# Performance work log

Measured on AMD Instinct MI355X. Metric: run time of the kernel, lower is better.

## Reference

```python
import jax, jax.numpy as jnp
import numpy as np

B, N, K = 4096, 87, 87


def setup_inputs() -> dict:
    key = jax.random.key(0)
    ks = jax.random.split(key, 6)
    x = jax.random.normal(ks[0], (B, N, N), dtype=jnp.float32)
    evals = jax.random.uniform(ks[1], (B, K), dtype=jnp.float32)
    evecs = jax.random.normal(ks[2], (B, N, K), dtype=jnp.float32)
    # learned per-node diffusion times (torch inits to 0, clamped to 1e-8;
    # use small positive values to exercise the exp decay)
    diffusion_time = jax.random.uniform(ks[3], (N,), dtype=jnp.float32) * 0.1
    # MiniMLP: single Linear(2*N -> N)
    lim = 1.0 / np.sqrt(2 * N)
    W = jax.random.uniform(ks[4], (N, 2 * N), minval=-lim, maxval=lim, dtype=jnp.float32)
    b = jax.random.uniform(ks[5], (N,), minval=-lim, maxval=lim, dtype=jnp.float32)
    return {"x": x, "evals": evals, "evecs": evecs,
            "diffusion_time": diffusion_time, "W": W, "b": b}


def reference(x, evals, evecs, diffusion_time, W, b):
    # clamp diffusion times (torch does this in-place on .data)
    t = jnp.maximum(diffusion_time, 1e-8)                     # (N,)
    # expa[b,i,m] = exp(-t_i * eval[b,m])
    expa = jnp.exp(-t[None, :, None] * evals[:, None, :])     # (B,N,K)
    # kernel[b,i,j] = sum_m evec[b,i,m] * expa[b,i,m] * evec[b,j,m]
    # (equivalent to the diag_embed + triple matmul + diagonal in the torch code)
    kernel = jnp.einsum('bim,bjm->bij', evecs * expa, evecs)  # (B,N,N)
    x_diffuse = jnp.concatenate([x, kernel], axis=2)          # (B,N,2N)
    return x_diffuse @ W.T + b                                # (B,N,N)
```

## Files before the change

kernel.cpp:

```cpp
#include <hip/hip_runtime.h>
#include <hip/hip_bf16.h>
#include <math.h>

#define NN    87
#define NN2   (NN * NN)
#define RP    96
#define SW    128
#define WPH   104
#define WPANEL (RP * WPH)
#define NT    256

#define WS_NEED (2 * WPANEL * 2)

typedef __attribute__((ext_vector_type(8))) short bf16x8;
typedef __attribute__((ext_vector_type(4))) short bf16x4;
typedef __attribute__((ext_vector_type(4))) float f32x4;
typedef float f32x4u __attribute__((ext_vector_type(4), aligned(4)));

__device__ __forceinline__ short f2bf(float f) {
    __hip_bfloat16 h = __float2bfloat16(f);
    return *(short*)&h;
}
__device__ __forceinline__ float bf2f(short s) {
    union { unsigned u; float f; } v;
    v.u = ((unsigned)(unsigned short)s) << 16;
    return v.f;
}

__device__ __forceinline__ int swz(int row, int col) {
    int m = ((row & 7) << 3) | (((row >> 3) & 1) << 2);
    return row * SW + (col ^ m);
}

__global__ void prep(const float* __restrict__ W, short* __restrict__ wp) {
    int idx = (int)blockIdx.x * NT + (int)threadIdx.x;
    if (idx >= 2 * WPANEL) return;
    int p = idx / WPANEL, rem = idx - p * WPANEL;
    int r = rem / WPH, c = rem - r * WPH;
    short v = 0;
    if (r < NN && c < NN) v = f2bf(W[r * (2 * NN) + p * NN + c]);
    wp[idx] = v;
}

template <bool WS>
__device__ __forceinline__ bf16x8 wload(const short* __restrict__ wp,
                                        const float* __restrict__ gW,
                                        int panel, int jrow, int jcl, int k0, bool tailKs)
{
    if constexpr (WS) {
        return *(const bf16x8*)&wp[panel * WPANEL + jrow * WPH + k0];
    } else {
        float v[8];
        if (!tailKs) {
            f32x4u a  = *(const f32x4u*)(gW + jcl * (2 * NN) + panel * NN + k0);
            f32x4u b4 = *(const f32x4u*)(gW + jcl * (2 * NN) + panel * NN + k0 + 4);
            v[0] = a.x; v[1] = a.y; v[2] = a.z; v[3] = a.w;
            v[4] = b4.x; v[5] = b4.y; v[6] = b4.z; v[7] = b4.w;
        } else {
            #pragma unroll
            for (int q = 0; q < 8; ++q) {
                int k = k0 + q;
                v[q] = (k < NN) ? gW[jcl * (2 * NN) + panel * NN + k] : 0.f;
            }
        }
        bf16x8 o;
        #pragma unroll
        for (int q = 0; q < 8; ++q) o[q] = f2bf(v[q]);
        return o;
    }
}

template <bool WS>
__global__ __launch_bounds__(NT, 3)
void fused(const float* __restrict__ gx, const float* __restrict__ gevals,
           const float* __restrict__ gevecs, const float* __restrict__ dtime,
           const float* __restrict__ gW, const float* __restrict__ bias,
           const short* __restrict__ wp, float* __restrict__ out)
{
    __shared__ __align__(16) short smem[2 * RP * SW];
    short* const sE = smem;
    short* const sX = smem + RP * SW;
    short* const sD = smem;
    float* const sF = (float*)smem;
    __shared__ float sLam[RP];

    const int b    = (int)blockIdx.x;
    const int tid  = (int)threadIdx.x;
    const int lane = tid & 63;
    const int wave = tid >> 6;
    const int l15  = lane & 15;
    const int lk   = lane >> 4;
    const int i0   = (wave >> 1) * 48;
    const int j0   = (wave & 1) * 48;

    const float* __restrict__ Eb   = gevecs + (size_t)b * NN2;
    const float* __restrict__ xb   = gx     + (size_t)b * NN2;
    const float* __restrict__ lamb = gevals + (size_t)b * NN;

    if (tid < RP) sLam[tid] = (tid < NN) ? lamb[tid] : 0.f;

    int ir[3], jr[3];
    float tr_[3];
    #pragma unroll
    for (int r = 0; r < 3; ++r) {
        ir[r] = i0 + 16 * r + l15;
        jr[r] = j0 + 16 * r + l15;
        tr_[r] = fmaxf(dtime[ir[r] < NN ? ir[r] : NN - 1], 1e-8f);
    }

    bf16x8 wfx[3][3];
    #pragma unroll
    for (int ks = 0; ks < 3; ++ks)
        #pragma unroll
        for (int wr = 0; wr < 3; ++wr) {
            int jc = jr[wr] < NN ? jr[wr] : NN - 1;
            wfx[ks][wr] = wload<WS>(wp, gW, 0, jr[wr], jc, ks * 32 + lk * 8, ks == 2);
        }

    for (int u = tid; u < NN * 22; u += NT) {
        int r = u / 22, sg = u - r * 22, c = sg * 4;
        const float* pE = Eb + r * NN + c;
        const float* pX = xb + r * NN + c;
        float e0, e1, e2, e3, x0, x1, x2, x3;
        if (sg < 21) {
            f32x4u te = *(const f32x4u*)pE; e0 = te.x; e1 = te.y; e2 = te.z; e3 = te.w;
            f32x4u tx = *(const f32x4u*)pX; x0 = tx.x; x1 = tx.y; x2 = tx.z; x3 = tx.w;
        } else {
            e0 = pE[0]; e1 = pE[1]; e2 = pE[2]; e3 = 0.f;
            x0 = pX[0]; x1 = pX[1]; x2 = pX[2]; x3 = 0.f;
        }
        bf16x4 we = {f2bf(e0), f2bf(e1), f2bf(e2), f2bf(e3)};
        bf16x4 wx = {f2bf(x0), f2bf(x1), f2bf(x2), f2bf(x3)};
        *(bf16x4*)&sE[swz(r, c)] = we;
        *(bf16x4*)&sX[swz(r, c)] = wx;
    }
    {
        const bf16x4 z = {0, 0, 0, 0};
        for (int u = tid; u < 9 * 24; u += NT) {
            int r = NN + u / 24, c = (u % 24) * 4;
            *(bf16x4*)&sE[swz(r, c)] = z;
            *(bf16x4*)&sX[swz(r, c)] = z;
        }
        for (int u = tid; u < NN * 2; u += NT) {
            int r = u >> 1, c = 88 + (u & 1) * 4;
            *(bf16x4*)&sE[swz(r, c)] = z;
            *(bf16x4*)&sX[swz(r, c)] = z;
        }
    }
    __syncthreads();

    f32x4 acc1[3][3];
    #pragma unroll
    for (int c = 0; c < 3; ++c)
        #pragma unroll
        for (int r = 0; r < 3; ++r) acc1[c][r] = (f32x4){0.f, 0.f, 0.f, 0.f};

    #pragma unroll
    for (int ks = 0; ks < 3; ++ks) {
        const int k0 = ks * 32 + lk * 8;
        f32x4 la  = *(const f32x4*)&sLam[k0];
        f32x4 lb4 = *(const f32x4*)&sLam[k0 + 4];
        float l8_[8] = {la.x, la.y, la.z, la.w, lb4.x, lb4.y, lb4.z, lb4.w};

        bf16x8 ef[3], af[3];
        #pragma unroll
        for (int c = 0; c < 3; ++c) {
            bf16x4 lo = *(const bf16x4*)&sE[swz(jr[c], k0)];
            bf16x4 hi = *(const bf16x4*)&sE[swz(jr[c], k0 + 4)];
            #pragma unroll
            for (int q = 0; q < 4; ++q) { ef[c][q] = lo[q]; ef[c][q + 4] = hi[q]; }
        }
        #pragma unroll
        for (int r = 0; r < 3; ++r) {
            bf16x4 lo = *(const bf16x4*)&sE[swz(ir[r], k0)];
            bf16x4 hi = *(const bf16x4*)&sE[swz(ir[r], k0 + 4)];
            #pragma unroll
            for (int q = 0; q < 4; ++q) {
                af[r][q]     = f2bf(bf2f(lo[q]) * __expf(-tr_[r] * l8_[q]));
                af[r][q + 4] = f2bf(bf2f(hi[q]) * __expf(-tr_[r] * l8_[q + 4]));
            }
        }
        #pragma unroll
        for (int c = 0; c < 3; ++c)
            #pragma unroll
            for (int r = 0; r < 3; ++r)
                acc1[c][r] = __builtin_amdgcn_mfma_f32_16x16x32_bf16(ef[c], af[r], acc1[c][r], 0, 0, 0);
    }
    __syncthreads();

    bf16x8 wfd[3][3];
    #pragma unroll
    for (int ks = 0; ks < 3; ++ks)
        #pragma unroll
        for (int wr = 0; wr < 3; ++wr) {
            int jc = jr[wr] < NN ? jr[wr] : NN - 1;
            wfd[ks][wr] = wload<WS>(wp, gW, 1, jr[wr], jc, ks * 32 + lk * 8, ks == 2);
        }

    #pragma unroll
    for (int c = 0; c < 3; ++c) {
        const int jb = j0 + 16 * c + lk * 4;
        #pragma unroll
        for (int r = 0; r < 3; ++r) {
            const int i = i0 + 16 * r + l15;
            bf16x4 v = {f2bf(acc1[c][r][0]), f2bf(acc1[c][r][1]),
                        f2bf(acc1[c][r][2]), f2bf(acc1[c][r][3])};
            *(bf16x4*)&sD[swz(i, jb)] = v;
        }
    }
    __builtin_amdgcn_sched_barrier(0);

    f32x4 acc2[3][3];
    #pragma unroll
    for (int wr = 0; wr < 3; ++wr)
        #pragma unroll
        for (int xc = 0; xc < 3; ++xc) acc2[wr][xc] = (f32x4){0.f, 0.f, 0.f, 0.f};

    #pragma unroll
    for (int ks = 0; ks < 3; ++ks) {
        const int k0 = ks * 32 + lk * 8;
        bf16x8 xf[3];
        #pragma unroll
        for (int xc = 0; xc < 3; ++xc) {
            bf16x4 lo = *(const bf16x4*)&sX[swz(ir[xc], k0)];
            bf16x4 hi = *(const bf16x4*)&sX[swz(ir[xc], k0 + 4)];
            #pragma unroll
            for (int q = 0; q < 4; ++q) { xf[xc][q] = lo[q]; xf[xc][q + 4] = hi[q]; }
        }
        #pragma unroll
        for (int wr = 0; wr < 3; ++wr)
            #pragma unroll
            for (int xc = 0; xc < 3; ++xc)
                acc2[wr][xc] = __builtin_amdgcn_mfma_f32_16x16x32_bf16(wfx[ks][wr], xf[xc], acc2[wr][xc], 0, 0, 0);
    }
    __syncthreads();

    #pragma unroll
    for (int ks = 0; ks < 3; ++ks) {
        const int k0 = ks * 32 + lk * 8;
        bf16x8 df[3];
        #pragma unroll
        for (int xc = 0; xc < 3; ++xc) {
            bf16x4 lo = *(const bf16x4*)&sD[swz(ir[xc], k0)];
            bf16x4 hi = *(const bf16x4*)&sD[swz(ir[xc], k0 + 4)];
            #pragma unroll
            for (int q = 0; q < 4; ++q) { df[xc][q] = lo[q]; df[xc][q + 4] = hi[q]; }
        }
        #pragma unroll
        for (int wr = 0; wr < 3; ++wr)
            #pragma unroll
            for (int xc = 0; xc < 3; ++xc)
                acc2[wr][xc] = __builtin_amdgcn_mfma_f32_16x16x32_bf16(wfd[ks][wr], df[xc], acc2[wr][xc], 0, 0, 0);
    }
    __syncthreads();

    #pragma unroll
    for (int wr = 0; wr < 3; ++wr) {
        const int jb = j0 + 16 * wr + lk * 4;
        float bj[4];
        if (jb + 3 < NN) {
            f32x4u t = *(const f32x4u*)(bias + jb);
            bj[0] = t.x; bj[1] = t.y; bj[2] = t.z; bj[3] = t.w;
        } else {
            #pragma unroll
            for (int q = 0; q < 4; ++q) bj[q] = (jb + q < NN) ? bias[jb + q] : 0.f;
        }
        #pragma unroll
        for (int xc = 0; xc < 3; ++xc) {
            const int i = i0 + 16 * xc + l15;
            #pragma unroll
            for (int q = 0; q < 4; ++q) {
                const int j = jb + q;
                if (j < NN) sF[i * NN + j] = acc2[wr][xc][q] + bj[q];
            }
        }
    }
    __syncthreads();

    {
        float* __restrict__ gb = out + (size_t)b * NN2;
        const int s = (4 - ((b * NN2) & 3)) & 3;
        if (tid < s) gb[tid] = sF[tid];
        const int C = (NN2 - s) >> 2;
        for (int m = tid; m < C; m += NT) {
            const int n = s + 4 * m;
            f32x4 v;
            v.x = sF[n]; v.y = sF[n + 1]; v.z = sF[n + 2]; v.w = sF[n + 3];
            *(f32x4*)(gb + n) = v;
        }
        const int tl = s + 4 * C;
        if (tid < NN2 - tl) gb[tl + tid] = sF[tl + tid];
    }
}

extern "C" void kernel_launch(void* const* d_in, const int* in_sizes, int n_in,
                              void* d_out, int out_size, void* d_ws, size_t ws_size,
                              hipStream_t stream)
{
    const float* x     = (const float*)d_in[0];
    const float* evals = (const float*)d_in[1];
    const float* evecs = (const float*)d_in[2];
    const float* dtime = (const float*)d_in[3];
    const float* W     = (const float*)d_in[4];
    const float* bias  = (const float*)d_in[5];
    float* out = (float*)d_out;

    const int B = in_sizes[1] / NN;

    if (ws_size >= (size_t)WS_NEED) {
        short* wp = (short*)d_ws;
        prep<<<(2 * WPANEL + NT - 1) / NT, NT, 0, stream>>>(W, wp);
        fused<true><<<dim3(B), dim3(NT), 0, stream>>>(x, evals, evecs, dtime, W, bias, wp, out);
    } else {
        fused<false><<<dim3(B), dim3(NT), 0, stream>>>(x, evals, evecs, dtime, W, bias, nullptr, out);
    }
}
```

Baseline: 106.1 us.

## Stream evecs directly into LDS as fp32 and overlap x loads with GEMM

```diff
diff --git a/kernel.cpp b/kernel.cpp
--- a/kernel.cpp
+++ b/kernel.cpp
@@ -4,13 +4,18 @@
 
 #define NN    87
 #define NN2   (NN * NN)
-#define RP    96
-#define SW    128
+#define EPW   92
+#define EPN   (96 * EPW + 4)
+#define XPW   92
+#define XPN   (96 * XPW + 16)
 #define WPH   104
-#define WPANEL (RP * WPH)
+#define WPANEL (96 * WPH)
 #define NT    256
 
-#define WS_NEED (2 * WPANEL * 2)
+#define WS_W     0
+#define WS_EPAD  (2 * WPANEL * 2)
+#define EPAD_N   8360
+#define WS_NEED  (WS_EPAD + EPAD_N * 4)
 
 typedef __attribute__((ext_vector_type(8))) short bf16x8;
 typedef __attribute__((ext_vector_type(4))) short bf16x4;
@@ -21,25 +26,29 @@
     __hip_bfloat16 h = __float2bfloat16(f);
     return *(short*)&h;
 }
-__device__ __forceinline__ float bf2f(short s) {
-    union { unsigned u; float f; } v;
-    v.u = ((unsigned)(unsigned short)s) << 16;
-    return v.f;
-}
-
-__device__ __forceinline__ int swz(int row, int col) {
-    int m = ((row & 7) << 3) | (((row >> 3) & 1) << 2);
-    return row * SW + (col ^ m);
-}
-
-__global__ void prep(const float* __restrict__ W, short* __restrict__ wp) {
+
+__device__ __forceinline__ void gl16(const float* g, float* l) {
+    __builtin_amdgcn_global_load_lds(
+        (const __attribute__((address_space(1))) void*)g,
+        (__attribute__((address_space(3))) void*)l, 16, 0, 0);
+}
+
+__global__ void prep(const float* __restrict__ W, const float* __restrict__ evecs,
+                     int B, char* __restrict__ ws)
+{
     int idx = (int)blockIdx.x * NT + (int)threadIdx.x;
-    if (idx >= 2 * WPANEL) return;
-    int p = idx / WPANEL, rem = idx - p * WPANEL;
-    int r = rem / WPH, c = rem - r * WPH;
-    short v = 0;
-    if (r < NN && c < NN) v = f2bf(W[r * (2 * NN) + p * NN + c]);
-    wp[idx] = v;
+    short* wp = (short*)(ws + WS_W);
+    float* ep = (float*)(ws + WS_EPAD);
+    if (idx < 2 * WPANEL) {
+        int p = idx / WPANEL, rem = idx - p * WPANEL;
+        int r = rem / WPH, c = rem - r * WPH;
+        short v = 0;
+        if (r < NN && c < NN) v = f2bf(W[r * (2 * NN) + p * NN + c]);
+        wp[idx] = v;
+    }
+    int i2 = idx - 2 * WPANEL;
+    if (i2 >= 0 && i2 < EPAD_N)
+        ep[i2] = (i2 < NN2) ? evecs[(size_t)(B - 1) * NN2 + i2] : 0.f;
 }
 
 template <bool WS>
@@ -75,14 +84,13 @@
 void fused(const float* __restrict__ gx, const float* __restrict__ gevals,
            const float* __restrict__ gevecs, const float* __restrict__ dtime,
            const float* __restrict__ gW, const float* __restrict__ bias,
-           const short* __restrict__ wp, float* __restrict__ out)
+           const char* __restrict__ ws, int B, float* __restrict__ out)
 {
-    __shared__ __align__(16) short smem[2 * RP * SW];
-    short* const sE = smem;
-    short* const sX = smem + RP * SW;
-    short* const sD = smem;
-    float* const sF = (float*)smem;
-    __shared__ float sLam[RP];
+    __shared__ __align__(16) float sE[EPN];
+    __shared__ __align__(16) short sX[XPN];
+    __shared__ float sLam[96];
+    short* const sD = (short*)sE;
+    float* const sF = (float*)sE;
 
     const int b    = (int)blockIdx.x;
     const int tid  = (int)threadIdx.x;
@@ -93,11 +101,15 @@
     const int i0   = (wave >> 1) * 48;
     const int j0   = (wave & 1) * 48;
 
-    const float* __restrict__ Eb   = gevecs + (size_t)b * NN2;
-    const float* __restrict__ xb   = gx     + (size_t)b * NN2;
-    const float* __restrict__ lamb = gevals + (size_t)b * NN;
-
-    if (tid < RP) sLam[tid] = (tid < NN) ? lamb[tid] : 0.f;
+    const float* __restrict__ Eb = gevecs + (size_t)b * NN2;
+    const float* __restrict__ xb = gx     + (size_t)b * NN2;
+    const short* wp = nullptr;
+    if constexpr (WS) {
+        wp = (const short*)(ws + WS_W);
+        if (b == B - 1) Eb = (const float*)(ws + WS_EPAD);
+    }
+
+    if (tid < 96) sLam[tid] = (tid < NN) ? gevals[(size_t)b * NN + tid] : 3e38f;
 
     int ir[3], jr[3];
     float tr_[3];
@@ -108,46 +120,62 @@
         tr_[r] = fmaxf(dtime[ir[r] < NN ? ir[r] : NN - 1], 1e-8f);
     }
 
-    bf16x8 wfx[3][3];
-    #pragma unroll
-    for (int ks = 0; ks < 3; ++ks)
-        #pragma unroll
-        for (int wr = 0; wr < 3; ++wr) {
-            int jc = jr[wr] < NN ? jr[wr] : NN - 1;
-            wfx[ks][wr] = wload<WS>(wp, gW, 0, jr[wr], jc, ks * 32 + lk * 8, ks == 2);
-        }
-
-    for (int u = tid; u < NN * 22; u += NT) {
-        int r = u / 22, sg = u - r * 22, c = sg * 4;
-        const float* pE = Eb + r * NN + c;
-        const float* pX = xb + r * NN + c;
-        float e0, e1, e2, e3, x0, x1, x2, x3;
-        if (sg < 21) {
-            f32x4u te = *(const f32x4u*)pE; e0 = te.x; e1 = te.y; e2 = te.z; e3 = te.w;
-            f32x4u tx = *(const f32x4u*)pX; x0 = tx.x; x1 = tx.y; x2 = tx.z; x3 = tx.w;
-        } else {
-            e0 = pE[0]; e1 = pE[1]; e2 = pE[2]; e3 = 0.f;
-            x0 = pX[0]; x1 = pX[1]; x2 = pX[2]; x3 = 0.f;
-        }
-        bf16x4 we = {f2bf(e0), f2bf(e1), f2bf(e2), f2bf(e3)};
-        bf16x4 wx = {f2bf(x0), f2bf(x1), f2bf(x2), f2bf(x3)};
-        *(bf16x4*)&sE[swz(r, c)] = we;
-        *(bf16x4*)&sX[swz(r, c)] = wx;
-    }
-    {
-        const bf16x4 z = {0, 0, 0, 0};
-        for (int u = tid; u < 9 * 24; u += NT) {
-            int r = NN + u / 24, c = (u % 24) * 4;
-            *(bf16x4*)&sE[swz(r, c)] = z;
-            *(bf16x4*)&sX[swz(r, c)] = z;
-        }
-        for (int u = tid; u < NN * 2; u += NT) {
-            int r = u >> 1, c = 88 + (u & 1) * 4;
-            *(bf16x4*)&sE[swz(r, c)] = z;
-            *(bf16x4*)&sX[swz(r, c)] = z;
-        }
-    }
-    __syncthreads();
+    if (tid < 4)  sE[96 * EPW + tid] = 0.f;
+    if (tid < 16) sX[96 * XPW + tid] = 0;
+    for (int u = tid; u < 96 * 5; u += NT) {
+        int r = u / 5, c = NN + u % 5;
+        sX[r * XPW + c] = 0;
+    }
+    for (int u = tid; u < 9 * NN; u += NT) {
+        int r = NN + u / NN, c = u % NN;
+        sX[r * XPW + c] = 0;
+    }
+
+    if constexpr (WS) {
+        for (int vc = wave; vc < 35; vc += 4) {
+            int p  = vc * 256 + lane * 4;
+            int row = p / EPW;
+            int col = p - row * EPW;
+            const float* g = Eb + row * NN + col;
+            if (vc < 34) gl16(g, &sE[vc * 256]);
+            else if (lane < 32) gl16(g, &sE[vc * 256]);
+        }
+    } else {
+        for (int u = tid; u < NN * 22; u += NT) {
+            int r = u / 22, sg = u - r * 22, c = sg * 4;
+            const float* pE = Eb + r * NN + c;
+            if (sg < 21) *(f32x4*)&sE[r * EPW + c] = *(const f32x4u*)pE;
+            else { f32x4 t; t.x = pE[0]; t.y = pE[1]; t.z = pE[2]; t.w = 0.f;
+                   *(f32x4*)&sE[r * EPW + c] = t; }
+        }
+        for (int u = tid; u < 96 * 4; u += NT) {
+            int r = u >> 2, c = 88 + (u & 3);
+            sE[r * EPW + c] = 0.f;
+        }
+        for (int u = tid; u < 9 * 88; u += NT) {
+            int r = NN + u / 88, c = u % 88;
+            sE[r * EPW + c] = 0.f;
+        }
+    }
+
+    float xq[8][4];
+    float x7568 = 0.f;
+    #pragma unroll
+    for (int k = 0; k < 8; ++k) {
+        int u = tid + k * NT;
+        int uc = (u < 1892) ? u : 1891;
+        f32x4u t = *(const f32x4u*)(xb + 4 * uc);
+        xq[k][0] = t.x; xq[k][1] = t.y; xq[k][2] = t.z; xq[k][3] = t.w;
+    }
+    if (tid == 0) x7568 = xb[7568];
+
+    if constexpr (WS) {
+        asm volatile("s_waitcnt vmcnt(8) lgkmcnt(0)" ::: "memory");
+        __builtin_amdgcn_s_barrier();
+        __builtin_amdgcn_sched_barrier(0);
+    } else {
+        __syncthreads();
+    }
 
     f32x4 acc1[3][3];
     #pragma unroll
@@ -165,19 +193,19 @@
         bf16x8 ef[3], af[3];
         #pragma unroll
         for (int c = 0; c < 3; ++c) {
-            bf16x4 lo = *(const bf16x4*)&sE[swz(jr[c], k0)];
-            bf16x4 hi = *(const bf16x4*)&sE[swz(jr[c], k0 + 4)];
-            #pragma unroll
-            for (int q = 0; q < 4; ++q) { ef[c][q] = lo[q]; ef[c][q + 4] = hi[q]; }
+            f32x4 lo = *(const f32x4*)&sE[jr[c] * EPW + k0];
+            f32x4 hi = *(const f32x4*)&sE[jr[c] * EPW + k0 + 4];
+            #pragma unroll
+            for (int q = 0; q < 4; ++q) { ef[c][q] = f2bf(lo[q]); ef[c][q + 4] = f2bf(hi[q]); }
         }
         #pragma unroll
         for (int r = 0; r < 3; ++r) {
-            bf16x4 lo = *(const bf16x4*)&sE[swz(ir[r], k0)];
-            bf16x4 hi = *(const bf16x4*)&sE[swz(ir[r], k0 + 4)];
+            f32x4 lo = *(const f32x4*)&sE[ir[r] * EPW + k0];
+            f32x4 hi = *(const f32x4*)&sE[ir[r] * EPW + k0 + 4];
             #pragma unroll
             for (int q = 0; q < 4; ++q) {
-                af[r][q]     = f2bf(bf2f(lo[q]) * __expf(-tr_[r] * l8_[q]));
-                af[r][q + 4] = f2bf(bf2f(hi[q]) * __expf(-tr_[r] * l8_[q + 4]));
+                af[r][q]     = f2bf(lo[q] * __expf(-tr_[r] * l8_[q]));
+                af[r][q + 4] = f2bf(hi[q] * __expf(-tr_[r] * l8_[q + 4]));
             }
         }
         #pragma unroll
@@ -188,27 +216,49 @@
     }
     __syncthreads();
 
-    bf16x8 wfd[3][3];
+    #pragma unroll
+    for (int c = 0; c < 3; ++c) {
+        const int jb = j0 + 16 * c + lk * 4;
+        if (jb < 92) {
+            #pragma unroll
+            for (int r = 0; r < 3; ++r) {
+                const int i = i0 + 16 * r + l15;
+                bf16x4 v = {f2bf(acc1[c][r][0]), f2bf(acc1[c][r][1]),
+                            f2bf(acc1[c][r][2]), f2bf(acc1[c][r][3])};
+                *(bf16x4*)&sD[i * XPW + jb] = v;
+            }
+        }
+    }
+    if (tid < 4) sD[96 * XPW + tid] = 0;
+    __builtin_amdgcn_sched_barrier(0);
+
+    #pragma unroll
+    for (int k = 0; k < 8; ++k) {
+        int u = tid + k * NT;
+        if (u < 1892) {
+            int f = 4 * u;
+            #pragma unroll
+            for (int e = 0; e < 4; ++e) {
+                int fe = f + e;
+                if (fe < NN2) {
+                    int r = fe / NN, c = fe - r * NN;
+                    sX[r * XPW + c] = f2bf(xq[k][e]);
+                }
+            }
+        }
+    }
+    if (tid == 0) sX[86 * XPW + 86] = f2bf(x7568);
+
+    bf16x8 wfx[3][3], wfd[3][3];
     #pragma unroll
     for (int ks = 0; ks < 3; ++ks)
         #pragma unroll
         for (int wr = 0; wr < 3; ++wr) {
             int jc = jr[wr] < NN ? jr[wr] : NN - 1;
+            wfx[ks][wr] = wload<WS>(wp, gW, 0, jr[wr], jc, ks * 32 + lk * 8, ks == 2);
             wfd[ks][wr] = wload<WS>(wp, gW, 1, jr[wr], jc, ks * 32 + lk * 8, ks == 2);
         }
-
-    #pragma unroll
-    for (int c = 0; c < 3; ++c) {
-        const int jb = j0 + 16 * c + lk * 4;
-        #pragma unroll
-        for (int r = 0; r < 3; ++r) {
-            const int i = i0 + 16 * r + l15;
-            bf16x4 v = {f2bf(acc1[c][r][0]), f2bf(acc1[c][r][1]),
-                        f2bf(acc1[c][r][2]), f2bf(acc1[c][r][3])};
-            *(bf16x4*)&sD[swz(i, jb)] = v;
-        }
-    }
-    __builtin_amdgcn_sched_barrier(0);
+    __syncthreads();
 
     f32x4 acc2[3][3];
     #pragma unroll
@@ -222,8 +272,8 @@
         bf16x8 xf[3];
         #pragma unroll
         for (int xc = 0; xc < 3; ++xc) {
-            bf16x4 lo = *(const bf16x4*)&sX[swz(ir[xc], k0)];
-            bf16x4 hi = *(const bf16x4*)&sX[swz(ir[xc], k0 + 4)];
+            bf16x4 lo = *(const bf16x4*)&sX[ir[xc] * XPW + k0];
+            bf16x4 hi = *(const bf16x4*)&sX[ir[xc] * XPW + k0 + 4];
             #pragma unroll
             for (int q = 0; q < 4; ++q) { xf[xc][q] = lo[q]; xf[xc][q + 4] = hi[q]; }
         }
@@ -233,16 +283,14 @@
             for (int xc = 0; xc < 3; ++xc)
                 acc2[wr][xc] = __builtin_amdgcn_mfma_f32_16x16x32_bf16(wfx[ks][wr], xf[xc], acc2[wr][xc], 0, 0, 0);
     }
-    __syncthreads();
-
     #pragma unroll
     for (int ks = 0; ks < 3; ++ks) {
         const int k0 = ks * 32 + lk * 8;
         bf16x8 df[3];
         #pragma unroll
         for (int xc = 0; xc < 3; ++xc) {
-            bf16x4 lo = *(const bf16x4*)&sD[swz(ir[xc], k0)];
-            bf16x4 hi = *(const bf16x4*)&sD[swz(ir[xc], k0 + 4)];
+            bf16x4 lo = *(const bf16x4*)&sD[ir[xc] * XPW + k0];
+            bf16x4 hi = *(const bf16x4*)&sD[ir[xc] * XPW + k0 + 4];
             #pragma unroll
             for (int q = 0; q < 4; ++q) { df[xc][q] = lo[q]; df[xc][q + 4] = hi[q]; }
         }
@@ -308,10 +356,12 @@
     const int B = in_sizes[1] / NN;
 
     if (ws_size >= (size_t)WS_NEED) {
-        short* wp = (short*)d_ws;
-        prep<<<(2 * WPANEL + NT - 1) / NT, NT, 0, stream>>>(W, wp);
-        fused<true><<<dim3(B), dim3(NT), 0, stream>>>(x, evals, evecs, dtime, W, bias, wp, out);
+        const int prep_elems = 2 * WPANEL + EPAD_N;
+        prep<<<(prep_elems + NT - 1) / NT, NT, 0, stream>>>(W, evecs, B, (char*)d_ws);
+        fused<true><<<dim3(B), dim3(NT), 0, stream>>>(x, evals, evecs, dtime, W, bias,
+                                                      (const char*)d_ws, B, out);
     } else {
-        fused<false><<<dim3(B), dim3(NT), 0, stream>>>(x, evals, evecs, dtime, W, bias, nullptr, out);
-    }
-}
+        fused<false><<<dim3(B), dim3(NT), 0, stream>>>(x, evals, evecs, dtime, W, bias,
+                                                       nullptr, B, out);
+    }
+}
```

After: 96.00 us. 9.5% less time.

## Shrink LDS with padded unswizzled tiles, batch global loads, raise occupancy to 4

Applied to the files above, without the earlier changes.

```diff
diff --git a/kernel.cpp b/kernel.cpp
--- a/kernel.cpp
+++ b/kernel.cpp
@@ -4,10 +4,10 @@
 
 #define NN    87
 #define NN2   (NN * NN)
-#define RP    96
-#define SW    128
+#define PW    92
+#define PN    (96 * PW + 16)
 #define WPH   104
-#define WPANEL (RP * WPH)
+#define WPANEL (96 * WPH)
 #define NT    256
 
 #define WS_NEED (2 * WPANEL * 2)
@@ -25,11 +25,6 @@
     union { unsigned u; float f; } v;
     v.u = ((unsigned)(unsigned short)s) << 16;
     return v.f;
-}
-
-__device__ __forceinline__ int swz(int row, int col) {
-    int m = ((row & 7) << 3) | (((row >> 3) & 1) << 2);
-    return row * SW + (col ^ m);
 }
 
 __global__ void prep(const float* __restrict__ W, short* __restrict__ wp) {
@@ -71,18 +66,18 @@
 }
 
 template <bool WS>
-__global__ __launch_bounds__(NT, 3)
+__global__ __launch_bounds__(NT, 4)
 void fused(const float* __restrict__ gx, const float* __restrict__ gevals,
            const float* __restrict__ gevecs, const float* __restrict__ dtime,
            const float* __restrict__ gW, const float* __restrict__ bias,
            const short* __restrict__ wp, float* __restrict__ out)
 {
-    __shared__ __align__(16) short smem[2 * RP * SW];
+    __shared__ __align__(16) short smem[2 * PN];
     short* const sE = smem;
-    short* const sX = smem + RP * SW;
+    short* const sX = smem + PN;
     short* const sD = smem;
     float* const sF = (float*)smem;
-    __shared__ float sLam[RP];
+    __shared__ float sLam[96];
 
     const int b    = (int)blockIdx.x;
     const int tid  = (int)threadIdx.x;
@@ -93,11 +88,11 @@
     const int i0   = (wave >> 1) * 48;
     const int j0   = (wave & 1) * 48;
 
-    const float* __restrict__ Eb   = gevecs + (size_t)b * NN2;
-    const float* __restrict__ xb   = gx     + (size_t)b * NN2;
-    const float* __restrict__ lamb = gevals + (size_t)b * NN;
-
-    if (tid < RP) sLam[tid] = (tid < NN) ? lamb[tid] : 0.f;
+    const float* __restrict__ Eb = gevecs + (size_t)b * NN2;
+    const float* __restrict__ xb = gx     + (size_t)b * NN2;
+    const short* wpp = WS ? wp : nullptr;
+
+    if (tid < 96) sLam[tid] = (tid < NN) ? gevals[(size_t)b * NN + tid] : 3e38f;
 
     int ir[3], jr[3];
     float tr_[3];
@@ -108,43 +103,47 @@
         tr_[r] = fmaxf(dtime[ir[r] < NN ? ir[r] : NN - 1], 1e-8f);
     }
 
-    bf16x8 wfx[3][3];
-    #pragma unroll
-    for (int ks = 0; ks < 3; ++ks)
-        #pragma unroll
-        for (int wr = 0; wr < 3; ++wr) {
-            int jc = jr[wr] < NN ? jr[wr] : NN - 1;
-            wfx[ks][wr] = wload<WS>(wp, gW, 0, jr[wr], jc, ks * 32 + lk * 8, ks == 2);
-        }
-
-    for (int u = tid; u < NN * 22; u += NT) {
-        int r = u / 22, sg = u - r * 22, c = sg * 4;
+    float ve[8][4], vx[8][4];
+    #pragma unroll
+    for (int k = 0; k < 8; ++k) {
+        int u = tid + k * NT;
+        int uu = (u < 1914) ? u : 0;
+        int r = uu / 22, sg = uu - r * 22, c = sg * 4;
         const float* pE = Eb + r * NN + c;
         const float* pX = xb + r * NN + c;
-        float e0, e1, e2, e3, x0, x1, x2, x3;
         if (sg < 21) {
-            f32x4u te = *(const f32x4u*)pE; e0 = te.x; e1 = te.y; e2 = te.z; e3 = te.w;
-            f32x4u tx = *(const f32x4u*)pX; x0 = tx.x; x1 = tx.y; x2 = tx.z; x3 = tx.w;
+            f32x4u te = *(const f32x4u*)pE;
+            ve[k][0] = te.x; ve[k][1] = te.y; ve[k][2] = te.z; ve[k][3] = te.w;
+            f32x4u tx = *(const f32x4u*)pX;
+            vx[k][0] = tx.x; vx[k][1] = tx.y; vx[k][2] = tx.z; vx[k][3] = tx.w;
         } else {
-            e0 = pE[0]; e1 = pE[1]; e2 = pE[2]; e3 = 0.f;
-            x0 = pX[0]; x1 = pX[1]; x2 = pX[2]; x3 = 0.f;
-        }
-        bf16x4 we = {f2bf(e0), f2bf(e1), f2bf(e2), f2bf(e3)};
-        bf16x4 wx = {f2bf(x0), f2bf(x1), f2bf(x2), f2bf(x3)};
-        *(bf16x4*)&sE[swz(r, c)] = we;
-        *(bf16x4*)&sX[swz(r, c)] = wx;
-    }
+            ve[k][0] = pE[0]; ve[k][1] = pE[1]; ve[k][2] = pE[2]; ve[k][3] = 0.f;
+            vx[k][0] = pX[0]; vx[k][1] = pX[1]; vx[k][2] = pX[2]; vx[k][3] = 0.f;
+        }
+    }
+
     {
         const bf16x4 z = {0, 0, 0, 0};
-        for (int u = tid; u < 9 * 24; u += NT) {
-            int r = NN + u / 24, c = (u % 24) * 4;
-            *(bf16x4*)&sE[swz(r, c)] = z;
-            *(bf16x4*)&sX[swz(r, c)] = z;
-        }
-        for (int u = tid; u < NN * 2; u += NT) {
-            int r = u >> 1, c = 88 + (u & 1) * 4;
-            *(bf16x4*)&sE[swz(r, c)] = z;
-            *(bf16x4*)&sX[swz(r, c)] = z;
+        for (int u = tid; u < 596; u += NT) {
+            int p = u & 1, v = u >> 1;
+            short* P = p ? sX : sE;
+            int off;
+            if (v < 207)      { int r = 87 + v / 23, s = v % 23; off = r * PW + s * 4; }
+            else if (v < 294) { off = (v - 207) * PW + 88; }
+            else              { off = 96 * PW + (v - 294) * 4; }
+            *(bf16x4*)&P[off] = z;
+        }
+    }
+
+    #pragma unroll
+    for (int k = 0; k < 8; ++k) {
+        int u = tid + k * NT;
+        if (u < 1914) {
+            int r = u / 22, sg = u - r * 22, c = sg * 4;
+            bf16x4 we = {f2bf(ve[k][0]), f2bf(ve[k][1]), f2bf(ve[k][2]), f2bf(ve[k][3])};
+            bf16x4 wx = {f2bf(vx[k][0]), f2bf(vx[k][1]), f2bf(vx[k][2]), f2bf(vx[k][3])};
+            *(bf16x4*)&sE[r * PW + c] = we;
+            *(bf16x4*)&sX[r * PW + c] = wx;
         }
     }
     __syncthreads();
@@ -165,15 +164,15 @@
         bf16x8 ef[3], af[3];
         #pragma unroll
         for (int c = 0; c < 3; ++c) {
-            bf16x4 lo = *(const bf16x4*)&sE[swz(jr[c], k0)];
-            bf16x4 hi = *(const bf16x4*)&sE[swz(jr[c], k0 + 4)];
+            bf16x4 lo = *(const bf16x4*)&sE[jr[c] * PW + k0];
+            bf16x4 hi = *(const bf16x4*)&sE[jr[c] * PW + k0 + 4];
             #pragma unroll
             for (int q = 0; q < 4; ++q) { ef[c][q] = lo[q]; ef[c][q + 4] = hi[q]; }
         }
         #pragma unroll
         for (int r = 0; r < 3; ++r) {
-            bf16x4 lo = *(const bf16x4*)&sE[swz(ir[r], k0)];
-            bf16x4 hi = *(const bf16x4*)&sE[swz(ir[r], k0 + 4)];
+            bf16x4 lo = *(const bf16x4*)&sE[ir[r] * PW + k0];
+            bf16x4 hi = *(const bf16x4*)&sE[ir[r] * PW + k0 + 4];
             #pragma unroll
             for (int q = 0; q < 4; ++q) {
                 af[r][q]     = f2bf(bf2f(lo[q]) * __expf(-tr_[r] * l8_[q]));
@@ -188,27 +187,30 @@
     }
     __syncthreads();
 
-    bf16x8 wfd[3][3];
+    bf16x8 wfx[3][3];
     #pragma unroll
     for (int ks = 0; ks < 3; ++ks)
         #pragma unroll
         for (int wr = 0; wr < 3; ++wr) {
             int jc = jr[wr] < NN ? jr[wr] : NN - 1;
-            wfd[ks][wr] = wload<WS>(wp, gW, 1, jr[wr], jc, ks * 32 + lk * 8, ks == 2);
+            wfx[ks][wr] = wload<WS>(wpp, gW, 0, jr[wr], jc, ks * 32 + lk * 8, ks == 2);
         }
 
     #pragma unroll
     for (int c = 0; c < 3; ++c) {
         const int jb = j0 + 16 * c + lk * 4;
-        #pragma unroll
-        for (int r = 0; r < 3; ++r) {
-            const int i = i0 + 16 * r + l15;
-            bf16x4 v = {f2bf(acc1[c][r][0]), f2bf(acc1[c][r][1]),
-                        f2bf(acc1[c][r][2]), f2bf(acc1[c][r][3])};
-            *(bf16x4*)&sD[swz(i, jb)] = v;
+        if (jb < PW) {
+            #pragma unroll
+            for (int r = 0; r < 3; ++r) {
+                const int i = i0 + 16 * r + l15;
+                bf16x4 v = {f2bf(acc1[c][r][0]), f2bf(acc1[c][r][1]),
+                            f2bf(acc1[c][r][2]), f2bf(acc1[c][r][3])};
+                *(bf16x4*)&sD[i * PW + jb] = v;
+            }
         }
     }
     __builtin_amdgcn_sched_barrier(0);
+    __syncthreads();
 
     f32x4 acc2[3][3];
     #pragma unroll
@@ -222,8 +224,8 @@
         bf16x8 xf[3];
         #pragma unroll
         for (int xc = 0; xc < 3; ++xc) {
-            bf16x4 lo = *(const bf16x4*)&sX[swz(ir[xc], k0)];
-            bf16x4 hi = *(const bf16x4*)&sX[swz(ir[xc], k0 + 4)];
+            bf16x4 lo = *(const bf16x4*)&sX[ir[xc] * PW + k0];
+            bf16x4 hi = *(const bf16x4*)&sX[ir[xc] * PW + k0 + 4];
             #pragma unroll
             for (int q = 0; q < 4; ++q) { xf[xc][q] = lo[q]; xf[xc][q + 4] = hi[q]; }
         }
@@ -233,16 +235,19 @@
             for (int xc = 0; xc < 3; ++xc)
                 acc2[wr][xc] = __builtin_amdgcn_mfma_f32_16x16x32_bf16(wfx[ks][wr], xf[xc], acc2[wr][xc], 0, 0, 0);
     }
-    __syncthreads();
-
     #pragma unroll
     for (int ks = 0; ks < 3; ++ks) {
         const int k0 = ks * 32 + lk * 8;
-        bf16x8 df[3];
+        bf16x8 wfd[3], df[3];
+        #pragma unroll
+        for (int wr = 0; wr < 3; ++wr) {
+            int jc = jr[wr] < NN ? jr[wr] : NN - 1;
+            wfd[wr] = wload<WS>(wpp, gW, 1, jr[wr], jc, k0, ks == 2);
+        }
         #pragma unroll
         for (int xc = 0; xc < 3; ++xc) {
-            bf16x4 lo = *(const bf16x4*)&sD[swz(ir[xc], k0)];
-            bf16x4 hi = *(const bf16x4*)&sD[swz(ir[xc], k0 + 4)];
+            bf16x4 lo = *(const bf16x4*)&sD[ir[xc] * PW + k0];
+            bf16x4 hi = *(const bf16x4*)&sD[ir[xc] * PW + k0 + 4];
             #pragma unroll
             for (int q = 0; q < 4; ++q) { df[xc][q] = lo[q]; df[xc][q + 4] = hi[q]; }
         }
@@ -250,7 +255,7 @@
         for (int wr = 0; wr < 3; ++wr)
             #pragma unroll
             for (int xc = 0; xc < 3; ++xc)
-                acc2[wr][xc] = __builtin_amdgcn_mfma_f32_16x16x32_bf16(wfd[ks][wr], df[xc], acc2[wr][xc], 0, 0, 0);
+                acc2[wr][xc] = __builtin_amdgcn_mfma_f32_16x16x32_bf16(wfd[wr], df[xc], acc2[wr][xc], 0, 0, 0);
     }
     __syncthreads();
 
```

After: 101.9 us. 4.0% less time.
